# Optimization experiments

Hardware: AMD Instinct MI355X
Metric: run time of the kernel (lower is better)

The kernel has to match this reference:

```python
import jax, jax.numpy as jnp
import numpy as np

B, IN, H = 4096, 1024, 1024


def setup_inputs() -> dict:
    key = jax.random.key(0)
    ks = jax.random.split(key, 16)
    s = 1.0 / np.sqrt(IN)
    inp = {
        "x_t": jax.random.normal(ks[0], (B, IN), jnp.float32),
        "h_prev": jax.random.normal(ks[1], (B, H), jnp.float32),
        "c_prev": jax.random.normal(ks[2], (B, H), jnp.float32),
        "W_xi": jax.random.uniform(ks[3], (H, IN), jnp.float32, -s, s),
        "W_hi": jax.random.normal(ks[4], (H, H), jnp.float32) / np.sqrt(H),
        "b_i": jnp.zeros((H,), jnp.float32),
        "W_xf": jax.random.uniform(ks[5], (H, IN), jnp.float32, -s, s),
        "W_hf": jax.random.normal(ks[6], (H, H), jnp.float32) / np.sqrt(H),
        "b_f": jnp.ones((H,), jnp.float32),
        "W_xg": jax.random.uniform(ks[7], (H, IN), jnp.float32, -s, s),
        "W_hg": jax.random.normal(ks[8], (H, H), jnp.float32) / np.sqrt(H),
        "b_g": jnp.zeros((H,), jnp.float32),
        "W_xo": jax.random.uniform(ks[9], (H, IN), jnp.float32, -s, s),
        "W_ho": jax.random.normal(ks[10], (H, H), jnp.float32) / np.sqrt(H),
        "b_o": jnp.zeros((H,), jnp.float32),
    }
    return inp


def reference(x_t, h_prev, c_prev,
              W_xi, W_hi, b_i,
              W_xf, W_hf, b_f,
              W_xg, W_hg, b_g,
              W_xo, W_ho, b_o):
    # i/f/g/o gates: sigmoid/sigmoid/tanh/sigmoid of (x W_x^T + h W_h^T + b)
    i_t = jax.nn.sigmoid(x_t @ W_xi.T + h_prev @ W_hi.T + b_i)
    f_t = jax.nn.sigmoid(x_t @ W_xf.T + h_prev @ W_hf.T + b_f)
    g_t = jnp.tanh(x_t @ W_xg.T + h_prev @ W_hg.T + b_g)
    o_t = jax.nn.sigmoid(x_t @ W_xo.T + h_prev @ W_ho.T + b_o)
    c_t = f_t * c_prev + i_t * g_t
    h_t = o_t * jnp.tanh(c_t)
    return (h_t, c_t)
```

## Files before the change

kernel.cpp:

```cpp
#include <hip/hip_runtime.h>
#include <hip/hip_bf16.h>


constexpr int Mdim = 4096;
constexpr int Ndim = 4096;
constexpr int Kdim = 2048;
constexpr int Hdim = 1024;
constexpr int BM = 128;
constexpr int BN = 128;
constexpr int BK = 64;
constexpr int NT = Kdim / BK;

using short8 = __attribute__((ext_vector_type(8))) short;
using f32x4  = __attribute__((ext_vector_type(4))) float;

__device__ __forceinline__ float sigmoid_(float x) {
    return 1.f / (1.f + __expf(-x));
}
__device__ __forceinline__ float tanh_(float x) {
    float e = __expf(2.f * x);
    return (e - 1.f) / (e + 1.f);
}

__global__ void build_AB(const float* __restrict__ x, const float* __restrict__ h,
                         const float* __restrict__ Wxi, const float* __restrict__ Whi,
                         const float* __restrict__ Wxf, const float* __restrict__ Whf,
                         const float* __restrict__ Wxg, const float* __restrict__ Whg,
                         const float* __restrict__ Wxo, const float* __restrict__ Who,
                         __hip_bfloat16* __restrict__ A, __hip_bfloat16* __restrict__ B) {
    int bidx = blockIdx.x;
    const float* src;
    __hip_bfloat16* dst;
    int idx = (bidx & 4095) * 256 + threadIdx.x;
    int row = idx >> 8;
    int c8  = (idx & 255) * 8;
    if (bidx < 4096) {
        src = (c8 < 1024) ? (x + (size_t)row * 1024 + c8)
                          : (h + (size_t)row * 1024 + (c8 - 1024));
        dst = A + (size_t)row * Kdim + c8;
    } else {
        int g = (row >> 4) & 3;
        int j = ((row >> 6) << 4) | (row & 15);
        const float* Wx = (g == 0) ? Wxi : (g == 1) ? Wxf : (g == 2) ? Wxg : Wxo;
        const float* Wh = (g == 0) ? Whi : (g == 1) ? Whf : (g == 2) ? Whg : Who;
        src = (c8 < 1024) ? (Wx + (size_t)j * 1024 + c8)
                          : (Wh + (size_t)j * 1024 + (c8 - 1024));
        dst = B + (size_t)row * Kdim + c8;
    }
    float4 f0 = ((const float4*)src)[0];
    float4 f1 = ((const float4*)src)[1];
    union { short8 v; __hip_bfloat16 e[8]; } u;
    u.e[0] = __float2bfloat16(f0.x); u.e[1] = __float2bfloat16(f0.y);
    u.e[2] = __float2bfloat16(f0.z); u.e[3] = __float2bfloat16(f0.w);
    u.e[4] = __float2bfloat16(f1.x); u.e[5] = __float2bfloat16(f1.y);
    u.e[6] = __float2bfloat16(f1.z); u.e[7] = __float2bfloat16(f1.w);
    *(short8*)dst = u.v;
}

#define RD(p) (*(const short8*)(p))

__launch_bounds__(256, 4)
__global__ void lstm_gemm(const __hip_bfloat16* __restrict__ A,
                          const __hip_bfloat16* __restrict__ B,
                          const float* __restrict__ c_prev,
                          const float* __restrict__ b_i, const float* __restrict__ b_f,
                          const float* __restrict__ b_g, const float* __restrict__ b_o,
                          float* __restrict__ out_h, float* __restrict__ out_c) {
    __shared__ __hip_bfloat16 As[128 * 64];
    __shared__ __hip_bfloat16 Bs[128 * 64];

    const int tid  = threadIdx.x;
    const int lane = tid & 63;
    const int w    = tid >> 6;
    const int wr   = w >> 1;
    const int wc   = w & 1;
    const int l15  = lane & 15, lhi = lane >> 4;

    int bid = blockIdx.x;
    int swz = (bid & 7) * 128 + (bid >> 3);
    const int bm = (swz >> 5) * BM;
    const int bn = (swz & 31) * BN;

    const int srow_  = tid >> 3;
    const int schunk = ((tid & 7) ^ ((tid >> 3) & 7)) * 8;

    const int swz4 = (l15 & 7) << 4;

#define STG1(dstbase, byteoff, srcptr, grow, kcol)                              \
    __builtin_amdgcn_global_load_lds(                                           \
        (const __attribute__((address_space(1))) unsigned*)(                    \
            (srcptr) + (size_t)((grow) + srow_) * Kdim + (kcol) + schunk),      \
        (__attribute__((address_space(3))) unsigned*)(                          \
            (char*)(dstbase) + (byteoff) + tid * 16), 16, 0, 0)

#define STAGE_TILE(kc)                                                          \
    do {                                                                        \
        STG1(As, 0,     A, bm + 0,  kc);                                        \
        STG1(As, 4096,  A, bm + 32, kc);                                        \
        STG1(As, 8192,  A, bm + 64, kc);                                        \
        STG1(As, 12288, A, bm + 96, kc);                                        \
        STG1(Bs, 0,     B, bn + 0,  kc);                                        \
        STG1(Bs, 4096,  B, bn + 32, kc);                                        \
        STG1(Bs, 8192,  B, bn + 64, kc);                                        \
        STG1(Bs, 12288, B, bn + 96, kc);                                        \
    } while (0)

    f32x4 acc[4][4];
#pragma unroll
    for (int a = 0; a < 4; ++a)
#pragma unroll
        for (int b = 0; b < 4; ++b)
            acc[a][b] = (f32x4){0.f, 0.f, 0.f, 0.f};

    STAGE_TILE(0);
    __builtin_amdgcn_sched_barrier(0);
    asm volatile("s_waitcnt vmcnt(0)" ::: "memory");
    __builtin_amdgcn_s_barrier();

    for (int t = 0; t < NT; ++t) {
#pragma unroll
        for (int kk = 0; kk < 2; ++kk) {
            const int kof = (kk * 64 + lhi * 16) ^ swz4;
            short8 af[4], bf[4];
#pragma unroll
            for (int a = 0; a < 4; ++a)
                af[a] = RD((const char*)As + (wr * 64 + a * 16 + l15) * 128 + kof);
#pragma unroll
            for (int b = 0; b < 4; ++b)
                bf[b] = RD((const char*)Bs + (wc * 64 + b * 16 + l15) * 128 + kof);
            __builtin_amdgcn_s_setprio(1);
#pragma unroll
            for (int a = 0; a < 4; ++a)
#pragma unroll
                for (int b = 0; b < 4; ++b)
                    acc[a][b] = __builtin_amdgcn_mfma_f32_16x16x32_bf16(
                        af[a], bf[b], acc[a][b], 0, 0, 0);
            __builtin_amdgcn_s_setprio(0);
        }

        if (t + 1 < NT) {
            __builtin_amdgcn_s_barrier();
            STAGE_TILE((t + 1) * BK);
            __builtin_amdgcn_sched_barrier(0);
            asm volatile("s_waitcnt vmcnt(0)" ::: "memory");
            __builtin_amdgcn_s_barrier();
        }
    }
#undef STG1
#undef STAGE_TILE

    const int j0 = ((bn + wc * 64) >> 6) * 16 + l15;
    const float bi  = b_i[j0];
    const float bf_ = b_f[j0];
    const float bg  = b_g[j0];
    const float bo  = b_o[j0];

#pragma unroll
    for (int a = 0; a < 4; ++a) {
        int mbase = bm + wr * 64 + a * 16 + lhi * 4;
#pragma unroll
        for (int r = 0; r < 4; ++r) {
            int m = mbase + r;
            float vi = acc[a][0][r] + bi;
            float vf = acc[a][1][r] + bf_;
            float vg = acc[a][2][r] + bg;
            float vo = acc[a][3][r] + bo;
            float it = sigmoid_(vi);
            float ft = sigmoid_(vf);
            float gt = tanh_(vg);
            float ot = sigmoid_(vo);
            float cp = c_prev[(size_t)m * Hdim + j0];
            float ct = ft * cp + it * gt;
            float ht = ot * tanh_(ct);
            out_h[(size_t)m * Hdim + j0] = ht;
            out_c[(size_t)m * Hdim + j0] = ct;
        }
    }
}

extern "C" void kernel_launch(void* const* d_in, const int* in_sizes, int n_in,
                              void* d_out, int out_size, void* d_ws, size_t ws_size,
                              hipStream_t stream) {
    const float* x_t    = (const float*)d_in[0];
    const float* h_prev = (const float*)d_in[1];
    const float* c_prev = (const float*)d_in[2];
    const float* W_xi   = (const float*)d_in[3];
    const float* W_hi   = (const float*)d_in[4];
    const float* b_i    = (const float*)d_in[5];
    const float* W_xf   = (const float*)d_in[6];
    const float* W_hf   = (const float*)d_in[7];
    const float* b_f    = (const float*)d_in[8];
    const float* W_xg   = (const float*)d_in[9];
    const float* W_hg   = (const float*)d_in[10];
    const float* b_g    = (const float*)d_in[11];
    const float* W_xo   = (const float*)d_in[12];
    const float* W_ho   = (const float*)d_in[13];
    const float* b_o    = (const float*)d_in[14];

    float* out_h = (float*)d_out;
    float* out_c = out_h + (size_t)Mdim * Hdim;

    __hip_bfloat16* Abf = (__hip_bfloat16*)d_ws;
    __hip_bfloat16* Bbf = Abf + (size_t)Mdim * Kdim;

    build_AB<<<8192, 256, 0, stream>>>(x_t, h_prev, W_xi, W_hi, W_xf, W_hf,
                                       W_xg, W_hg, W_xo, W_ho, Abf, Bbf);

    lstm_gemm<<<dim3((Mdim / BM) * (Ndim / BN)), 256, 0, stream>>>(
        Abf, Bbf, c_prev, b_i, b_f, b_g, b_o, out_h, out_c);
}
```

Measured before the change: 92.51 us.

## Widen GEMM tile to 128x256 with 512 threads and double-buffer B in LDS

The fused LSTM GEMM block grows to 512 threads in 8 waves covering a 128x256 output tile, which halves the grid and raises reuse of each A tile. The B tile is double-buffered in LDS and the next B slice is issued before the current slice's MFMAs, so its global loads overlap compute. A is still single-buffered and loaded after a barrier. LDS use rises to about 80 KB per block, which cuts resident blocks per CU, and the wait on all outstanding loads still blocks on the prefetched B.

Measured after the change: 88.93 us. 3.9% less time.

```diff
diff --git a/kernel.cpp b/kernel.cpp
--- a/kernel.cpp
+++ b/kernel.cpp
@@ -7,7 +7,7 @@
 constexpr int Kdim = 2048;
 constexpr int Hdim = 1024;
 constexpr int BM = 128;
-constexpr int BN = 128;
+constexpr int BN = 256;
 constexpr int BK = 64;
 constexpr int NT = Kdim / BK;
 
@@ -59,7 +59,7 @@
 
 #define RD(p) (*(const short8*)(p))
 
-__launch_bounds__(256, 4)
+__launch_bounds__(512, 4)
 __global__ void lstm_gemm(const __hip_bfloat16* __restrict__ A,
                           const __hip_bfloat16* __restrict__ B,
                           const float* __restrict__ c_prev,
@@ -67,19 +67,19 @@
                           const float* __restrict__ b_g, const float* __restrict__ b_o,
                           float* __restrict__ out_h, float* __restrict__ out_c) {
     __shared__ __hip_bfloat16 As[128 * 64];
-    __shared__ __hip_bfloat16 Bs[128 * 64];
+    __shared__ __hip_bfloat16 Bs[2][256 * 64];
 
     const int tid  = threadIdx.x;
     const int lane = tid & 63;
     const int w    = tid >> 6;
-    const int wr   = w >> 1;
-    const int wc   = w & 1;
+    const int wr   = w >> 2;
+    const int wc   = w & 3;
     const int l15  = lane & 15, lhi = lane >> 4;
 
     int bid = blockIdx.x;
-    int swz = (bid & 7) * 128 + (bid >> 3);
-    const int bm = (swz >> 5) * BM;
-    const int bn = (swz & 31) * BN;
+    int swz = (bid & 7) * 64 + (bid >> 3);
+    const int bm = (swz >> 4) * BM;
+    const int bn = (swz & 15) * BN;
 
     const int srow_  = tid >> 3;
     const int schunk = ((tid & 7) ^ ((tid >> 3) & 7)) * 8;
@@ -93,16 +93,18 @@
         (__attribute__((address_space(3))) unsigned*)(                          \
             (char*)(dstbase) + (byteoff) + tid * 16), 16, 0, 0)
 
-#define STAGE_TILE(kc)                                                          \
+#define STAGE_B(s, kc)                                                          \
     do {                                                                        \
-        STG1(As, 0,     A, bm + 0,  kc);                                        \
-        STG1(As, 4096,  A, bm + 32, kc);                                        \
-        STG1(As, 8192,  A, bm + 64, kc);                                        \
-        STG1(As, 12288, A, bm + 96, kc);                                        \
-        STG1(Bs, 0,     B, bn + 0,  kc);                                        \
-        STG1(Bs, 4096,  B, bn + 32, kc);                                        \
-        STG1(Bs, 8192,  B, bn + 64, kc);                                        \
-        STG1(Bs, 12288, B, bn + 96, kc);                                        \
+        STG1(&Bs[s][0], 0,     B, bn + 0,   kc);                                \
+        STG1(&Bs[s][0], 8192,  B, bn + 64,  kc);                                \
+        STG1(&Bs[s][0], 16384, B, bn + 128, kc);                                \
+        STG1(&Bs[s][0], 24576, B, bn + 192, kc);                                \
+    } while (0)
+
+#define STAGE_A(kc)                                                             \
+    do {                                                                        \
+        STG1(As, 0,    A, bm + 0,  kc);                                         \
+        STG1(As, 8192, A, bm + 64, kc);                                         \
     } while (0)
 
     f32x4 acc[4][4];
@@ -112,12 +114,17 @@
         for (int b = 0; b < 4; ++b)
             acc[a][b] = (f32x4){0.f, 0.f, 0.f, 0.f};
 
-    STAGE_TILE(0);
+    STAGE_A(0);
+    STAGE_B(0, 0);
     __builtin_amdgcn_sched_barrier(0);
     asm volatile("s_waitcnt vmcnt(0)" ::: "memory");
     __builtin_amdgcn_s_barrier();
 
     for (int t = 0; t < NT; ++t) {
+        const int d = t & 1;
+
+        if (t + 1 < NT) STAGE_B(d ^ 1, (t + 1) * BK);
+
 #pragma unroll
         for (int kk = 0; kk < 2; ++kk) {
             const int kof = (kk * 64 + lhi * 16) ^ swz4;
@@ -127,7 +134,7 @@
                 af[a] = RD((const char*)As + (wr * 64 + a * 16 + l15) * 128 + kof);
 #pragma unroll
             for (int b = 0; b < 4; ++b)
-                bf[b] = RD((const char*)Bs + (wc * 64 + b * 16 + l15) * 128 + kof);
+                bf[b] = RD((const char*)&Bs[d][0] + (wc * 64 + b * 16 + l15) * 128 + kof);
             __builtin_amdgcn_s_setprio(1);
 #pragma unroll
             for (int a = 0; a < 4; ++a)
@@ -139,15 +146,18 @@
         }
 
         if (t + 1 < NT) {
+            __builtin_amdgcn_sched_barrier(0);
+            asm volatile("s_waitcnt lgkmcnt(0)" ::: "memory");
             __builtin_amdgcn_s_barrier();
-            STAGE_TILE((t + 1) * BK);
+            STAGE_A((t + 1) * BK);
             __builtin_amdgcn_sched_barrier(0);
             asm volatile("s_waitcnt vmcnt(0)" ::: "memory");
             __builtin_amdgcn_s_barrier();
         }
     }
 #undef STG1
-#undef STAGE_TILE
+#undef STAGE_A
+#undef STAGE_B
 
     const int j0 = ((bn + wc * 64) >> 6) * 16 + l15;
     const float bi  = b_i[j0];
@@ -206,6 +216,6 @@
     build_AB<<<8192, 256, 0, stream>>>(x_t, h_prev, W_xi, W_hi, W_xf, W_hf,
                                        W_xg, W_hg, W_xo, W_ho, Abf, Bbf);
 
-    lstm_gemm<<<dim3((Mdim / BM) * (Ndim / BN)), 256, 0, stream>>>(
+    lstm_gemm<<<dim3((Mdim / BM) * (Ndim / BN)), 512, 0, stream>>>(
         Abf, Bbf, c_prev, b_i, b_f, b_g, b_o, out_h, out_c);
 }
```
